# Kernel optimization log

Hardware: AMD Instinct MI355X
Metric: run time of the kernel (lower is better)

The kernel has to match this reference:

```python
import jax, jax.numpy as jnp
import numpy as np

# Loihi CUBA LIF neuron constants (netParams['neuron'])
V_TH_MANT = 80.0
THETA = V_TH_MANT * 64.0          # threshold in voltage units (vThMant << 6)
I_DECAY = 1024.0
V_DECAY = 128.0
REF_DELAY = 1.0
DECAY_U = 1.0 - I_DECAY / 4096.0  # current decay per step
DECAY_V = 1.0 - V_DECAY / 4096.0  # voltage decay per step
TAU_RHO = 1.0
SCALE_RHO = 1.0
POOL_W = 1.1 * V_TH_MANT          # SLAYER pool weight: one input spike -> 1.1*theta drive


@jax.custom_vjp
def spike_fn(v):
    # Heaviside spike with SLAYER surrogate gradient
    return (v >= THETA).astype(v.dtype)

def _spike_fwd(v):
    return spike_fn(v), v

def _spike_bwd(v, g):
    sur = (SCALE_RHO / THETA) * jnp.exp(-jnp.abs(v - THETA) / (TAU_RHO * THETA))
    return (g * sur,)

spike_fn.defvjp(_spike_fwd, _spike_bwd)


def spike_loihi(x):
    """Loihi LIF recurrence over last (time) axis. x: [..., T] weighted spikes."""
    shp = x.shape
    xt = jnp.moveaxis(x.reshape(-1, shp[-1]), -1, 0)  # [T, N]
    z = jnp.zeros(xt.shape[1], x.dtype)
    def step(carry, x_t):
        u, v, ref = carry
        u = u * DECAY_U + x_t * 64.0                  # current state (input scaled by 2^6)
        active = (ref <= 0).astype(x.dtype)
        v = (v * DECAY_V + u) * active                # voltage, clamped in refractory period
        s = spike_fn(v)
        ref = jnp.where(s > 0, REF_DELAY, jnp.maximum(ref - 1.0, 0.0))
        v = v * (1.0 - s)                             # reset on spike
        return (u, v, ref), s
    _, spikes = jax.lax.scan(step, (z, z, z), xt)
    return jnp.moveaxis(spikes, 0, -1).reshape(shp)


def delay_shift(x, d=1):
    # shift spikes forward in time by d steps (zero-pad at t=0)
    return jnp.pad(x, [(0, 0)] * (x.ndim - 1) + [(d, 0)])[..., :x.shape[-1]]


def conv2d_t(x, w):
    # x: [B,C,H,W,T], w: [O,I,k,k]; 2D 'SAME' conv applied independently per timestep
    B, C, H, W, T = x.shape
    xm = jnp.moveaxis(x, -1, 1).reshape(B * T, C, H, W)
    y = jax.lax.conv_general_dilated(xm, w, (1, 1), 'SAME',
                                     dimension_numbers=('NCHW', 'OIHW', 'NCHW'))
    O = w.shape[0]
    return jnp.moveaxis(y.reshape(B, T, O, H, W), 1, -1)


def sum_pool(x, k):
    # SLAYER pool = sum over kxk window * fixed weight (per timestep)
    y = jax.lax.reduce_window(x, 0.0, jax.lax.add,
                              (1, 1, k, k, 1), (1, 1, k, k, 1), 'VALID')
    return y * POOL_W


def setup_inputs() -> dict:
    key = jax.random.key(0)
    ks = jax.random.split(key, 5)
    B, T = 8, 128
    x = (jax.random.uniform(ks[0], (B, 2, 128, 128, T)) < 0.1).astype(jnp.float32)
    w1 = jax.random.normal(ks[1], (16, 2, 5, 5), jnp.float32) * 10.0 * 0.2   # weightScale=10
    w2 = jax.random.normal(ks[2], (32, 16, 3, 3), jnp.float32) * 50.0 * 0.2  # weightScale=50
    wf1 = jax.random.normal(ks[3], (512, 2048), jnp.float32) * 100.0 * 0.02  # dense default scale
    wf2 = jax.random.normal(ks[4], (11, 512), jnp.float32) * 100.0 * 0.02
    return {"x": x, "w1": w1, "w2": w2, "wf1": wf1, "wf2": wf2}


def reference(x, w1, w2, wf1, wf2):
    s = spike_loihi(sum_pool(x, 4))            # [B,2,32,32,T]
    s = delay_shift(s)
    s = spike_loihi(conv2d_t(s, w1))           # [B,16,32,32,T]
    s = delay_shift(s)
    s = spike_loihi(sum_pool(s, 2))            # [B,16,16,16,T]
    s = delay_shift(s)
    s = spike_loihi(conv2d_t(s, w2))           # [B,32,16,16,T]
    s = delay_shift(s)
    s = spike_loihi(sum_pool(s, 2))            # [B,32,8,8,T]
    B, T = s.shape[0], s.shape[-1]
    s = s.reshape(B, -1, T)                    # [B,2048,T]
    s = delay_shift(s)
    s = spike_loihi(jnp.einsum('bft,of->bot', s, wf1))  # [B,512,T]
    s = delay_shift(s)
    s = spike_loihi(jnp.einsum('bft,of->bot', s, wf2))  # [B,11,T]
    s = delay_shift(s)
    return s[:, :, None, None, :]              # [B,11,1,1,T]
```

## Files before the change

### kernel.cpp

```cpp
#include <hip/hip_runtime.h>

#define TT 128

#define DECAY_U 0.75f
#define DECAY_V 0.96875f
#define THETA   5120.0f
#define POOLW   88.0f

__device__ __forceinline__ void lif_step(float xt, float& u, float& v, int& refc, float& s) {
    u = __fadd_rn(__fmul_rn(u, DECAY_U), __fmul_rn(xt, 64.0f));
    float vn = __fadd_rn(__fmul_rn(v, DECAY_V), u);
    v = refc ? 0.0f : vn;
    s = (v >= THETA) ? 1.0f : 0.0f;
    if (s > 0.f) { refc = 1; v = 0.f; }
    else         { refc = refc > 0 ? refc - 1 : 0; }
}

__device__ __forceinline__ void lif_seq_lds(float* col, int stride) {
    float u = 0.f, v = 0.f;
    int refc = 0;
    #pragma unroll 16
    for (int t = 0; t < TT; ++t) {
        float s;
        lif_step(col[t * stride], u, v, refc, s);
        col[t * stride] = s;
    }
}

__global__ void wtrans_k(const float* __restrict__ w1, const float* __restrict__ w2,
                         float* __restrict__ wT1, float* __restrict__ wT2) {
    int i = blockIdx.x * 256 + threadIdx.x;
    if (i < 800) {
        int oc = i & 15;
        int r2 = i >> 4;
        int ky = r2 / 10;
        int rr = r2 - ky * 10;
        int kx = rr >> 1, c = rr & 1;
        wT1[i] = w1[oc*50 + c*25 + ky*5 + kx];
    }
    if (i < 4608) {
        int oc = i & 31;
        int c  = (i >> 5) & 15;
        int tap = i >> 9;
        wT2[i] = w2[oc*144 + c*9 + tap];
    }
}

__global__ void pool1_lif_k(const float* __restrict__ x, unsigned char* __restrict__ pk1) {
    __shared__ float sb[TT][3];
    int t = threadIdx.x & 127, c = threadIdx.x >> 7;
    int pos = blockIdx.x & 1023, b = blockIdx.x >> 10;
    int px = pos & 31, py = pos >> 5;
    const float* base = x + (size_t)((((b*2 + c)*128 + py*4)*128) + px*4) * 128 + t;
    float s = 0.f;
    #pragma unroll
    for (int dy = 0; dy < 4; ++dy)
        #pragma unroll
        for (int dx = 0; dx < 4; ++dx)
            s += base[(dy*128 + dx) * 128];
    sb[t][c] = s * POOLW;
    __syncthreads();
    if (threadIdx.x < 2) lif_seq_lds(&sb[0][threadIdx.x], 3);
    __syncthreads();
    if (threadIdx.x < 128) {
        unsigned int v = (sb[t][0] > 0.5f ? 1u : 0u) | (sb[t][1] > 0.5f ? 2u : 0u);
        pk1[(size_t)b * 131072 + (size_t)pos * 128 + t] = (unsigned char)v;
    }
}

__global__ __launch_bounds__(256) void conv1_gemm_k(const unsigned char* __restrict__ pk1,
                                                    const float* __restrict__ wT1,
                                                    unsigned short* __restrict__ pk2) {
    __shared__ float smem[4760];
    float* WS = smem;
    unsigned int* XN = (unsigned int*)(smem + 800);
    float* sb = smem;
    int tid = threadIdx.x;
    int ppair = blockIdx.x & 511, b = blockIdx.x >> 9;
    int py = ppair >> 4, px0 = (ppair & 15) * 2;
    const unsigned char* pp = pk1 + (size_t)b * 131072;

    #pragma unroll
    for (int i = 0; i < 4; ++i) {
        int e = tid + 256*i;
        if (e < 800) WS[e] = wT1[e];
    }
    #pragma unroll
    for (int i = 0; i < 15; ++i) {
        int e = tid + 256*i;
        int row = e >> 7, t = e & 127;
        int ky = row / 6, xc = row - ky*6;
        int iy = py + ky - 2, ix = px0 + xc - 2;
        bool vs = ((unsigned)iy < 32u) && ((unsigned)ix < 32u) && (t > 0);
        XN[row*132 + t] = vs ? (unsigned int)pp[(iy*32 + ix)*128 + t - 1] : 0u;
    }
    __syncthreads();

    int tg = tid & 31;
    int pos = (tid >> 5) & 1;
    int og = tid >> 6;
    float acc[4][4];
    #pragma unroll
    for (int i = 0; i < 4; ++i)
        #pragma unroll
        for (int j = 0; j < 4; ++j) acc[i][j] = 0.f;

    #pragma unroll 1
    for (int ky = 0; ky < 5; ++ky) {
        #pragma unroll
        for (int kx = 0; kx < 5; ++kx) {
            uint4 xw = *(const uint4*)&XN[(ky*6 + kx + pos)*132 + tg*4];
            #pragma unroll
            for (int c = 0; c < 2; ++c) {
                float4 wv = *(const float4*)&WS[(ky*10 + kx*2 + c)*16 + og*4];
                float x0 = (float)((xw.x >> c) & 1u);
                float x1 = (float)((xw.y >> c) & 1u);
                float x2 = (float)((xw.z >> c) & 1u);
                float x3 = (float)((xw.w >> c) & 1u);
                acc[0][0] = fmaf(wv.x, x0, acc[0][0]);
                acc[0][1] = fmaf(wv.x, x1, acc[0][1]);
                acc[0][2] = fmaf(wv.x, x2, acc[0][2]);
                acc[0][3] = fmaf(wv.x, x3, acc[0][3]);
                acc[1][0] = fmaf(wv.y, x0, acc[1][0]);
                acc[1][1] = fmaf(wv.y, x1, acc[1][1]);
                acc[1][2] = fmaf(wv.y, x2, acc[1][2]);
                acc[1][3] = fmaf(wv.y, x3, acc[1][3]);
                acc[2][0] = fmaf(wv.z, x0, acc[2][0]);
                acc[2][1] = fmaf(wv.z, x1, acc[2][1]);
                acc[2][2] = fmaf(wv.z, x2, acc[2][2]);
                acc[2][3] = fmaf(wv.z, x3, acc[2][3]);
                acc[3][0] = fmaf(wv.w, x0, acc[3][0]);
                acc[3][1] = fmaf(wv.w, x1, acc[3][1]);
                acc[3][2] = fmaf(wv.w, x2, acc[3][2]);
                acc[3][3] = fmaf(wv.w, x3, acc[3][3]);
            }
        }
    }
    __syncthreads();
    #pragma unroll
    for (int i = 0; i < 4; ++i)
        #pragma unroll
        for (int j = 0; j < 4; ++j)
            sb[(tg*4 + j)*33 + (og*4 + i)*2 + pos] = acc[i][j];
    __syncthreads();
    if (tid < 32) lif_seq_lds(&sb[tid], 33);
    __syncthreads();
    if (tid < 128) {
        int t = tid;
        #pragma unroll
        for (int p2 = 0; p2 < 2; ++p2) {
            unsigned int w = 0;
            #pragma unroll
            for (int oc = 0; oc < 16; ++oc)
                w |= (sb[t*33 + oc*2 + p2] > 0.5f ? 1u : 0u) << oc;
            int pos_out = py*32 + px0 + p2;
            pk2[(size_t)b * 131072 + (size_t)pos_out * 128 + t] = (unsigned short)w;
        }
    }
}

__global__ __launch_bounds__(256) void pool2pack_k(const unsigned short* __restrict__ pk2,
                                                   unsigned short* __restrict__ pk3) {
    __shared__ float sb[TT][17];
    int tid = threadIdx.x;
    int t = tid & 127, half = tid >> 7;
    int pos = blockIdx.x & 255, b = blockIdx.x >> 8;
    int px = pos & 15, py = pos >> 4;
    unsigned int w0 = 0, w1 = 0, w2 = 0, w3 = 0;
    if (t > 0) {
        const unsigned short* q = pk2 + (size_t)b * 131072 + (size_t)(py*2*32 + px*2) * 128 + (t - 1);
        w0 = q[0]; w1 = q[128]; w2 = q[32*128]; w3 = q[33*128];
    }
    #pragma unroll
    for (int j = 0; j < 8; ++j) {
        int c = half*8 + j;
        int cnt = ((w0 >> c) & 1) + ((w1 >> c) & 1) + ((w2 >> c) & 1) + ((w3 >> c) & 1);
        sb[t][c] = POOLW * (float)cnt;
    }
    __syncthreads();
    if (tid < 16) lif_seq_lds(&sb[0][tid], 17);
    __syncthreads();
    if (tid < 128) {
        unsigned int w = 0;
        #pragma unroll
        for (int c = 0; c < 16; ++c)
            w |= (sb[tid][c] > 0.5f ? 1u : 0u) << c;
        pk3[(size_t)b * 32768 + (size_t)pos * 128 + tid] = (unsigned short)w;
    }
}

__global__ __launch_bounds__(256) void conv2_gemm_k(const unsigned short* __restrict__ pk3,
                                                    const float* __restrict__ wT2,
                                                    unsigned int* __restrict__ pk4) {
    __shared__ float smem[5796];
    float* WS = smem;
    unsigned int* XL = (unsigned int*)(smem + 4608);
    float* sb = smem;
    int tid = threadIdx.x;
    int pos = blockIdx.x & 255, b = blockIdx.x >> 8;
    int px = pos & 15, py = pos >> 4;
    const unsigned short* pp = pk3 + (size_t)b * 32768;

    #pragma unroll
    for (int i = 0; i < 18; ++i)
        WS[tid + 256*i] = wT2[tid + 256*i];
    #pragma unroll
    for (int i = 0; i < 5; ++i) {
        int e = tid + 256*i;
        if (e < 1152) {
            int tap = e >> 7, t = e & 127;
            int ky = tap / 3, kx = tap - ky*3;
            int iy = py + ky - 1, ix = px + kx - 1;
            bool vs = ((unsigned)iy < 16u) && ((unsigned)ix < 16u) && (t > 0);
            XL[tap*132 + t] = vs ? (unsigned int)pp[(iy*16 + ix)*128 + t - 1] : 0u;
        }
    }
    __syncthreads();

    int tg = tid & 31;
    int og = tid >> 5;
    float acc[4][4];
    #pragma unroll
    for (int i = 0; i < 4; ++i)
        #pragma unroll
        for (int j = 0; j < 4; ++j) acc[i][j] = 0.f;

    #pragma unroll 1
    for (int tap = 0; tap < 9; ++tap) {
        uint4 xw = *(const uint4*)&XL[tap*132 + tg*4];
        #pragma unroll
        for (int c = 0; c < 16; ++c) {
            float4 wv = *(const float4*)&WS[tap*512 + c*32 + og*4];
            float x0 = (float)((xw.x >> c) & 1u);
            float x1 = (float)((xw.y >> c) & 1u);
            float x2 = (float)((xw.z >> c) & 1u);
            float x3 = (float)((xw.w >> c) & 1u);
            acc[0][0] = fmaf(wv.x, x0, acc[0][0]);
            acc[0][1] = fmaf(wv.x, x1, acc[0][1]);
            acc[0][2] = fmaf(wv.x, x2, acc[0][2]);
            acc[0][3] = fmaf(wv.x, x3, acc[0][3]);
            acc[1][0] = fmaf(wv.y, x0, acc[1][0]);
            acc[1][1] = fmaf(wv.y, x1, acc[1][1]);
            acc[1][2] = fmaf(wv.y, x2, acc[1][2]);
            acc[1][3] = fmaf(wv.y, x3, acc[1][3]);
            acc[2][0] = fmaf(wv.z, x0, acc[2][0]);
            acc[2][1] = fmaf(wv.z, x1, acc[2][1]);
            acc[2][2] = fmaf(wv.z, x2, acc[2][2]);
            acc[2][3] = fmaf(wv.z, x3, acc[2][3]);
            acc[3][0] = fmaf(wv.w, x0, acc[3][0]);
            acc[3][1] = fmaf(wv.w, x1, acc[3][1]);
            acc[3][2] = fmaf(wv.w, x2, acc[3][2]);
            acc[3][3] = fmaf(wv.w, x3, acc[3][3]);
        }
    }
    __syncthreads();
    #pragma unroll
    for (int i = 0; i < 4; ++i)
        #pragma unroll
        for (int j = 0; j < 4; ++j)
            sb[(tg*4 + j)*33 + og*4 + i] = acc[i][j];
    __syncthreads();
    if (tid < 32) lif_seq_lds(&sb[tid], 33);
    __syncthreads();
    if (tid < 128) {
        unsigned int w = 0;
        #pragma unroll
        for (int oc = 0; oc < 32; ++oc)
            w |= (sb[tid*33 + oc] > 0.5f ? 1u : 0u) << oc;
        pk4[(size_t)b * 32768 + (size_t)pos * 128 + tid] = w;
    }
}

__global__ void pool3_lif_k(const unsigned int* __restrict__ pk4, float* __restrict__ s5) {
    __shared__ float sb[TT][3];
    int t = threadIdx.x & 127, pos = threadIdx.x >> 7;
    int n = blockIdx.x * 2 + pos;
    int px = n & 7, py = (n >> 3) & 7, c = (n >> 6) & 31, b = n >> 11;
    float acc = 0.f;
    if (t > 0) {
        const unsigned int* q = pk4 + (size_t)b * 32768 + (size_t)(py*2*16 + px*2) * 128 + (t - 1);
        unsigned int w0 = q[0], w1 = q[128], w2 = q[16*128], w3 = q[17*128];
        int cnt = ((w0 >> c) & 1) + ((w1 >> c) & 1) + ((w2 >> c) & 1) + ((w3 >> c) & 1);
        acc = POOLW * (float)cnt;
    }
    sb[t][pos] = acc;
    __syncthreads();
    if (threadIdx.x < 2) lif_seq_lds(&sb[0][threadIdx.x], 3);
    __syncthreads();
    s5[(size_t)n * TT + t] = sb[t][pos];
}

__global__ __launch_bounds__(256) void fc1_gemm_k(const float* __restrict__ s5,
                                                  const float* __restrict__ wf1,
                                                  float* __restrict__ part) {
    __shared__ float WT[64][68];
    __shared__ float ST[64][68];
    int bid = blockIdx.x;
    int kc = bid & 7;
    int ot = (bid >> 3) & 7;
    int tt = (bid >> 6) & 1;
    int b  = bid >> 7;
    int tid = threadIdx.x;
    int oo = tid >> 4;
    int to = tid & 15;

    const float* wbase = wf1 + (size_t)(ot*64) * 2048 + kc*256;
    const float* sbase = s5 + (size_t)b * 262144 + (size_t)(kc*256) * 128;

    float acc[4][4];
    #pragma unroll
    for (int i = 0; i < 4; ++i)
        #pragma unroll
        for (int j = 0; j < 4; ++j) acc[i][j] = 0.f;

    for (int ks = 0; ks < 4; ++ks) {
        __syncthreads();
        #pragma unroll
        for (int i = 0; i < 16; ++i) {
            int e = tid + 256*i;
            int o = e >> 6, f = e & 63;
            WT[f][o] = wbase[(size_t)o * 2048 + ks*64 + f];
        }
        #pragma unroll
        for (int i = 0; i < 16; ++i) {
            int e = tid + 256*i;
            int f = e >> 6, tl = e & 63;
            int tsrc = tt*64 + tl - 1;
            ST[f][tl] = (tsrc < 0) ? 0.f : sbase[(size_t)f * 128 + ks*64*128 + tsrc];
        }
        __syncthreads();
        #pragma unroll 4
        for (int k = 0; k < 64; ++k) {
            float4 a = *(const float4*)&WT[k][oo*4];
            float4 s = *(const float4*)&ST[k][to*4];
            acc[0][0] = fmaf(a.x, s.x, acc[0][0]);
            acc[0][1] = fmaf(a.x, s.y, acc[0][1]);
            acc[0][2] = fmaf(a.x, s.z, acc[0][2]);
            acc[0][3] = fmaf(a.x, s.w, acc[0][3]);
            acc[1][0] = fmaf(a.y, s.x, acc[1][0]);
            acc[1][1] = fmaf(a.y, s.y, acc[1][1]);
            acc[1][2] = fmaf(a.y, s.z, acc[1][2]);
            acc[1][3] = fmaf(a.y, s.w, acc[1][3]);
            acc[2][0] = fmaf(a.z, s.x, acc[2][0]);
            acc[2][1] = fmaf(a.z, s.y, acc[2][1]);
            acc[2][2] = fmaf(a.z, s.z, acc[2][2]);
            acc[2][3] = fmaf(a.z, s.w, acc[2][3]);
            acc[3][0] = fmaf(a.w, s.x, acc[3][0]);
            acc[3][1] = fmaf(a.w, s.y, acc[3][1]);
            acc[3][2] = fmaf(a.w, s.z, acc[3][2]);
            acc[3][3] = fmaf(a.w, s.w, acc[3][3]);
        }
    }
    float* pb = part + (size_t)kc * 524288 + (size_t)b * 65536
              + (size_t)(ot*64 + oo*4) * 128 + tt*64 + to*4;
    #pragma unroll
    for (int i = 0; i < 4; ++i)
        #pragma unroll
        for (int j = 0; j < 4; ++j)
            pb[(size_t)i * 128 + j] = acc[i][j];
}

__global__ void fc1_reduce_lif_k(const float* __restrict__ part, float* __restrict__ s6) {
    __shared__ float sb[TT][3];
    int t = threadIdx.x & 127, pos = threadIdx.x >> 7;
    int n = blockIdx.x * 2 + pos;
    float s = 0.f;
    #pragma unroll
    for (int kc = 0; kc < 8; ++kc)
        s += part[(size_t)kc * 524288 + (size_t)n * 128 + t];
    sb[t][pos] = s;
    __syncthreads();
    if (threadIdx.x < 2) lif_seq_lds(&sb[0][threadIdx.x], 3);
    __syncthreads();
    s6[(size_t)n * TT + t] = sb[t][pos];
}

__global__ void fc2_lif_k(const float* __restrict__ s6, const float* __restrict__ wf2,
                          float* __restrict__ out) {
    __shared__ float sb[TT];
    int t = threadIdx.x;
    int o = blockIdx.x % 11, b = blockIdx.x / 11;
    float acc = 0.f;
    if (t > 0) {
        const float* sp = s6 + (size_t)b * 65536 + (t - 1);
        const float* wp = wf2 + o * 512;
        for (int f = 0; f < 512; f += 4) {
            float4 w = *(const float4*)&wp[f];
            acc = fmaf(w.x, sp[(size_t)f * 128], acc);
            acc = fmaf(w.y, sp[(size_t)(f+1) * 128], acc);
            acc = fmaf(w.z, sp[(size_t)(f+2) * 128], acc);
            acc = fmaf(w.w, sp[(size_t)(f+3) * 128], acc);
        }
    }
    sb[t] = acc;
    __syncthreads();
    if (t == 0) lif_seq_lds(sb, 1);
    __syncthreads();
    float* q = out + (size_t)(b*11 + o) * TT;
    if (t == 0) q[0] = 0.f;
    if (t < TT - 1) q[t + 1] = sb[t];
}

extern "C" void kernel_launch(void* const* d_in, const int* in_sizes, int n_in,
                              void* d_out, int out_size, void* d_ws, size_t ws_size,
                              hipStream_t stream) {
    const float* x   = (const float*)d_in[0];
    const float* w1  = (const float*)d_in[1];
    const float* w2  = (const float*)d_in[2];
    const float* wf1 = (const float*)d_in[3];
    const float* wf2 = (const float*)d_in[4];
    float* out = (float*)d_out;

    float* ws = (float*)d_ws;
    float* PART = ws;
    float* A    = PART + 4194304;
    float* S6   = A + 2097152;
    float* WT1  = S6 + 524288;
    float* WT2  = WT1 + 800;
    unsigned char*  PK1 = (unsigned char*)(WT2 + 4608);
    unsigned short* PK2 = (unsigned short*)(PK1 + 1048576);
    unsigned short* PK3 = (unsigned short*)((char*)PK2 + 2097152);
    unsigned int*   PK4 = (unsigned int*)((char*)PK3 + 524288);

    wtrans_k<<<dim3(18), 256, 0, stream>>>(w1, w2, WT1, WT2);
    pool1_lif_k<<<dim3(8192), 256, 0, stream>>>(x, PK1);
    conv1_gemm_k<<<dim3(4096), 256, 0, stream>>>(PK1, WT1, PK2);
    pool2pack_k<<<dim3(2048), 256, 0, stream>>>(PK2, PK3);
    conv2_gemm_k<<<dim3(2048), 256, 0, stream>>>(PK3, WT2, PK4);
    pool3_lif_k<<<dim3(8192), 256, 0, stream>>>(PK4, A);
    fc1_gemm_k      <<<dim3(1024), 256, 0, stream>>>(A, wf1, PART);
    fc1_reduce_lif_k<<<dim3(2048), 256, 0, stream>>>(PART, S6);
    fc2_lif_k<<<dim3(88), 128, 0, stream>>>(S6, wf2, out);
}
```

Baseline: 213.5 us.

## Process two output positions per conv2 block and fully unroll tap loops

The conv2 kernel now computes two spatial positions per block, halving the grid. Each thread accumulates 8 output channels instead of 4, and the staged weight tile is reused across both positions. The LIF scan runs on 64 threads instead of 32. The tap loops in conv1 and conv2 are now fully unrolled. The intent is to amortise the per-block weight load into LDS and add ILP, at the cost of more registers (32 accumulators) and more shared memory per block, which may lower occupancy.

```diff
diff --git a/kernel.cpp b/kernel.cpp
--- a/kernel.cpp
+++ b/kernel.cpp
@@ -105,7 +105,7 @@
         #pragma unroll
         for (int j = 0; j < 4; ++j) acc[i][j] = 0.f;
 
-    #pragma unroll 1
+    #pragma unroll
     for (int ky = 0; ky < 5; ++ky) {
         #pragma unroll
         for (int kx = 0; kx < 5; ++kx) {
@@ -192,82 +192,107 @@
 __global__ __launch_bounds__(256) void conv2_gemm_k(const unsigned short* __restrict__ pk3,
                                                     const float* __restrict__ wT2,
                                                     unsigned int* __restrict__ pk4) {
-    __shared__ float smem[5796];
+    __shared__ float smem[8448];
     float* WS = smem;
     unsigned int* XL = (unsigned int*)(smem + 4608);
     float* sb = smem;
     int tid = threadIdx.x;
-    int pos = blockIdx.x & 255, b = blockIdx.x >> 8;
-    int px = pos & 15, py = pos >> 4;
+    int pp2 = blockIdx.x & 127, b = blockIdx.x >> 7;
     const unsigned short* pp = pk3 + (size_t)b * 32768;
 
     #pragma unroll
     for (int i = 0; i < 18; ++i)
         WS[tid + 256*i] = wT2[tid + 256*i];
     #pragma unroll
-    for (int i = 0; i < 5; ++i) {
+    for (int i = 0; i < 9; ++i) {
         int e = tid + 256*i;
-        if (e < 1152) {
-            int tap = e >> 7, t = e & 127;
-            int ky = tap / 3, kx = tap - ky*3;
-            int iy = py + ky - 1, ix = px + kx - 1;
-            bool vs = ((unsigned)iy < 16u) && ((unsigned)ix < 16u) && (t > 0);
-            XL[tap*132 + t] = vs ? (unsigned int)pp[(iy*16 + ix)*128 + t - 1] : 0u;
-        }
+        int pe2 = e >= 1152 ? 1 : 0;
+        int r = e - pe2*1152;
+        int tap = r >> 7, t = r & 127;
+        int pos_l = pp2*2 + pe2;
+        int px = pos_l & 15, py = pos_l >> 4;
+        int ky = tap / 3, kx = tap - ky*3;
+        int iy = py + ky - 1, ix = px + kx - 1;
+        bool vs = ((unsigned)iy < 16u) && ((unsigned)ix < 16u) && (t > 0);
+        XL[pe2*1188 + tap*132 + t] = vs ? (unsigned int)pp[(iy*16 + ix)*128 + t - 1] : 0u;
     }
     __syncthreads();
 
     int tg = tid & 31;
-    int og = tid >> 5;
-    float acc[4][4];
-    #pragma unroll
-    for (int i = 0; i < 4; ++i)
+    int og = (tid >> 5) & 3;
+    int pe = tid >> 7;
+    const unsigned int* XLp = XL + pe*1188;
+    float acc[8][4];
+    #pragma unroll
+    for (int i = 0; i < 8; ++i)
         #pragma unroll
         for (int j = 0; j < 4; ++j) acc[i][j] = 0.f;
 
-    #pragma unroll 1
+    #pragma unroll
     for (int tap = 0; tap < 9; ++tap) {
-        uint4 xw = *(const uint4*)&XL[tap*132 + tg*4];
+        uint4 xw = *(const uint4*)&XLp[tap*132 + tg*4];
         #pragma unroll
         for (int c = 0; c < 16; ++c) {
-            float4 wv = *(const float4*)&WS[tap*512 + c*32 + og*4];
+            float4 wv0 = *(const float4*)&WS[tap*512 + c*32 + og*8];
+            float4 wv1 = *(const float4*)&WS[tap*512 + c*32 + og*8 + 4];
             float x0 = (float)((xw.x >> c) & 1u);
             float x1 = (float)((xw.y >> c) & 1u);
             float x2 = (float)((xw.z >> c) & 1u);
             float x3 = (float)((xw.w >> c) & 1u);
-            acc[0][0] = fmaf(wv.x, x0, acc[0][0]);
-            acc[0][1] = fmaf(wv.x, x1, acc[0][1]);
-            acc[0][2] = fmaf(wv.x, x2, acc[0][2]);
-            acc[0][3] = fmaf(wv.x, x3, acc[0][3]);
-            acc[1][0] = fmaf(wv.y, x0, acc[1][0]);
-            acc[1][1] = fmaf(wv.y, x1, acc[1][1]);
-            acc[1][2] = fmaf(wv.y, x2, acc[1][2]);
-            acc[1][3] = fmaf(wv.y, x3, acc[1][3]);
-            acc[2][0] = fmaf(wv.z, x0, acc[2][0]);
-            acc[2][1] = fmaf(wv.z, x1, acc[2][1]);
-            acc[2][2] = fmaf(wv.z, x2, acc[2][2]);
-            acc[2][3] = fmaf(wv.z, x3, acc[2][3]);
-            acc[3][0] = fmaf(wv.w, x0, acc[3][0]);
-            acc[3][1] = fmaf(wv.w, x1, acc[3][1]);
-            acc[3][2] = fmaf(wv.w, x2, acc[3][2]);
-            acc[3][3] = fmaf(wv.w, x3, acc[3][3]);
-        }
-    }
-    __syncthreads();
-    #pragma unroll
-    for (int i = 0; i < 4; ++i)
+            acc[0][0] = fmaf(wv0.x, x0, acc[0][0]);
+            acc[0][1] = fmaf(wv0.x, x1, acc[0][1]);
+            acc[0][2] = fmaf(wv0.x, x2, acc[0][2]);
+            acc[0][3] = fmaf(wv0.x, x3, acc[0][3]);
+            acc[1][0] = fmaf(wv0.y, x0, acc[1][0]);
+            acc[1][1] = fmaf(wv0.y, x1, acc[1][1]);
+            acc[1][2] = fmaf(wv0.y, x2, acc[1][2]);
+            acc[1][3] = fmaf(wv0.y, x3, acc[1][3]);
+            acc[2][0] = fmaf(wv0.z, x0, acc[2][0]);
+            acc[2][1] = fmaf(wv0.z, x1, acc[2][1]);
+            acc[2][2] = fmaf(wv0.z, x2, acc[2][2]);
+            acc[2][3] = fmaf(wv0.z, x3, acc[2][3]);
+            acc[3][0] = fmaf(wv0.w, x0, acc[3][0]);
+            acc[3][1] = fmaf(wv0.w, x1, acc[3][1]);
+            acc[3][2] = fmaf(wv0.w, x2, acc[3][2]);
+            acc[3][3] = fmaf(wv0.w, x3, acc[3][3]);
+            acc[4][0] = fmaf(wv1.x, x0, acc[4][0]);
+            acc[4][1] = fmaf(wv1.x, x1, acc[4][1]);
+            acc[4][2] = fmaf(wv1.x, x2, acc[4][2]);
+            acc[4][3] = fmaf(wv1.x, x3, acc[4][3]);
+            acc[5][0] = fmaf(wv1.y, x0, acc[5][0]);
+            acc[5][1] = fmaf(wv1.y, x1, acc[5][1]);
+            acc[5][2] = fmaf(wv1.y, x2, acc[5][2]);
+            acc[5][3] = fmaf(wv1.y, x3, acc[5][3]);
+            acc[6][0] = fmaf(wv1.z, x0, acc[6][0]);
+            acc[6][1] = fmaf(wv1.z, x1, acc[6][1]);
+            acc[6][2] = fmaf(wv1.z, x2, acc[6][2]);
+            acc[6][3] = fmaf(wv1.z, x3, acc[6][3]);
+            acc[7][0] = fmaf(wv1.w, x0, acc[7][0]);
+            acc[7][1] = fmaf(wv1.w, x1, acc[7][1]);
+            acc[7][2] = fmaf(wv1.w, x2, acc[7][2]);
+            acc[7][3] = fmaf(wv1.w, x3, acc[7][3]);
+        }
+    }
+    __syncthreads();
+    float* sbp = sb + pe*4224;
+    #pragma unroll
+    for (int i = 0; i < 8; ++i)
         #pragma unroll
         for (int j = 0; j < 4; ++j)
-            sb[(tg*4 + j)*33 + og*4 + i] = acc[i][j];
-    __syncthreads();
-    if (tid < 32) lif_seq_lds(&sb[tid], 33);
-    __syncthreads();
-    if (tid < 128) {
+            sbp[(tg*4 + j)*33 + og*8 + i] = acc[i][j];
+    __syncthreads();
+    if (tid < 64) {
+        int pe_l = tid >> 5, oc_l = tid & 31;
+        lif_seq_lds(&sb[pe_l*4224 + oc_l], 33);
+    }
+    __syncthreads();
+    {
+        int t = tid & 127, pe_l = tid >> 7;
         unsigned int w = 0;
         #pragma unroll
         for (int oc = 0; oc < 32; ++oc)
-            w |= (sb[tid*33 + oc] > 0.5f ? 1u : 0u) << oc;
-        pk4[(size_t)b * 32768 + (size_t)pos * 128 + tid] = w;
+            w |= (sb[pe_l*4224 + t*33 + oc] > 0.5f ? 1u : 0u) << oc;
+        pk4[(size_t)b * 32768 + (size_t)(pp2*2 + pe_l) * 128 + t] = w;
     }
 }
 
@@ -426,7 +451,7 @@
     pool1_lif_k<<<dim3(8192), 256, 0, stream>>>(x, PK1);
     conv1_gemm_k<<<dim3(4096), 256, 0, stream>>>(PK1, WT1, PK2);
     pool2pack_k<<<dim3(2048), 256, 0, stream>>>(PK2, PK3);
-    conv2_gemm_k<<<dim3(2048), 256, 0, stream>>>(PK3, WT2, PK4);
+    conv2_gemm_k<<<dim3(1024), 256, 0, stream>>>(PK3, WT2, PK4);
     pool3_lif_k<<<dim3(8192), 256, 0, stream>>>(PK4, A);
     fc1_gemm_k      <<<dim3(1024), 256, 0, stream>>>(A, wf1, PART);
     fc1_reduce_lif_k<<<dim3(2048), 256, 0, stream>>>(PART, S6);
```

Result: faster. 203.1 us (-4.9%).

## Replace binary-spike conv GEMMs with precomputed weight-sum lookup tables

Applied to the files above, without the earlier changes.

Because the conv inputs are binary spikes, the change precomputes per-row (conv1, 10 bits) and per-tap-half (conv2, 8 bits) partial weight sums for every input bit pattern. Each thread then gathers these table rows and adds them instead of running bit-extract plus FMA loops over all channels and taps. This removes most of the arithmetic in both conv kernels. In exchange it adds a LUT build kernel, random gathers into an L2-resident table of roughly 900 KB, higher register pressure, and a different float summation order that can flip spikes near threshold.

```diff
diff --git a/kernel.cpp b/kernel.cpp
--- a/kernel.cpp
+++ b/kernel.cpp
@@ -27,22 +27,33 @@
     }
 }
 
-__global__ void wtrans_k(const float* __restrict__ w1, const float* __restrict__ w2,
-                         float* __restrict__ wT1, float* __restrict__ wT2) {
-    int i = blockIdx.x * 256 + threadIdx.x;
-    if (i < 800) {
-        int oc = i & 15;
-        int r2 = i >> 4;
-        int ky = r2 / 10;
-        int rr = r2 - ky * 10;
-        int kx = rr >> 1, c = rr & 1;
-        wT1[i] = w1[oc*50 + c*25 + ky*5 + kx];
-    }
-    if (i < 4608) {
-        int oc = i & 31;
-        int c  = (i >> 5) & 15;
-        int tap = i >> 9;
-        wT2[i] = w2[oc*144 + c*9 + tap];
+__global__ void lut_build_k(const float* __restrict__ w1, const float* __restrict__ w2,
+                            float* __restrict__ LUT1, float* __restrict__ LUT2) {
+    int id = blockIdx.x * 256 + threadIdx.x;
+    if (id < 81920) {
+        int ky = id >> 14;
+        int idx = (id >> 4) & 1023;
+        int oc = id & 15;
+        float s = 0.f;
+        #pragma unroll
+        for (int j = 0; j < 10; ++j)
+            if ((idx >> j) & 1) {
+                int kx = j >> 1, c = j & 1;
+                s += w1[oc*50 + c*25 + ky*5 + kx];
+            }
+        LUT1[id] = s;
+    }
+    if (id < 147456) {
+        int th = id >> 13;
+        int idx = (id >> 5) & 255;
+        int oc = id & 31;
+        int tap = th >> 1, half = th & 1;
+        float s = 0.f;
+        #pragma unroll
+        for (int j = 0; j < 8; ++j)
+            if ((idx >> j) & 1)
+                s += w2[oc*144 + (half*8 + j)*9 + tap];
+        LUT2[id] = s;
     }
 }
 
@@ -68,94 +79,57 @@
     }
 }
 
-__global__ __launch_bounds__(256) void conv1_gemm_k(const unsigned char* __restrict__ pk1,
-                                                    const float* __restrict__ wT1,
-                                                    unsigned short* __restrict__ pk2) {
-    __shared__ float smem[4760];
-    float* WS = smem;
-    unsigned int* XN = (unsigned int*)(smem + 800);
-    float* sb = smem;
-    int tid = threadIdx.x;
-    int ppair = blockIdx.x & 511, b = blockIdx.x >> 9;
-    int py = ppair >> 4, px0 = (ppair & 15) * 2;
+__global__ __launch_bounds__(128) void conv1_lut_k(const unsigned char* __restrict__ pk1,
+                                                   const float* __restrict__ LUT1,
+                                                   unsigned short* __restrict__ pk2) {
+    __shared__ float sb[TT*17];
+    int t = threadIdx.x;
+    int pos = blockIdx.x & 1023, b = blockIdx.x >> 10;
+    int px = pos & 31, py = pos >> 5;
     const unsigned char* pp = pk1 + (size_t)b * 131072;
 
-    #pragma unroll
-    for (int i = 0; i < 4; ++i) {
-        int e = tid + 256*i;
-        if (e < 800) WS[e] = wT1[e];
-    }
-    #pragma unroll
-    for (int i = 0; i < 15; ++i) {
-        int e = tid + 256*i;
-        int row = e >> 7, t = e & 127;
-        int ky = row / 6, xc = row - ky*6;
-        int iy = py + ky - 2, ix = px0 + xc - 2;
-        bool vs = ((unsigned)iy < 32u) && ((unsigned)ix < 32u) && (t > 0);
-        XN[row*132 + t] = vs ? (unsigned int)pp[(iy*32 + ix)*128 + t - 1] : 0u;
-    }
-    __syncthreads();
-
-    int tg = tid & 31;
-    int pos = (tid >> 5) & 1;
-    int og = tid >> 6;
-    float acc[4][4];
-    #pragma unroll
-    for (int i = 0; i < 4; ++i)
-        #pragma unroll
-        for (int j = 0; j < 4; ++j) acc[i][j] = 0.f;
-
-    #pragma unroll 1
+    unsigned int idx[5];
+    #pragma unroll
     for (int ky = 0; ky < 5; ++ky) {
+        int iy = py + ky - 2;
+        unsigned int v = 0;
         #pragma unroll
         for (int kx = 0; kx < 5; ++kx) {
-            uint4 xw = *(const uint4*)&XN[(ky*6 + kx + pos)*132 + tg*4];
-            #pragma unroll
-            for (int c = 0; c < 2; ++c) {
-                float4 wv = *(const float4*)&WS[(ky*10 + kx*2 + c)*16 + og*4];
-                float x0 = (float)((xw.x >> c) & 1u);
-                float x1 = (float)((xw.y >> c) & 1u);
-                float x2 = (float)((xw.z >> c) & 1u);
-                float x3 = (float)((xw.w >> c) & 1u);
-                acc[0][0] = fmaf(wv.x, x0, acc[0][0]);
-                acc[0][1] = fmaf(wv.x, x1, acc[0][1]);
-                acc[0][2] = fmaf(wv.x, x2, acc[0][2]);
-                acc[0][3] = fmaf(wv.x, x3, acc[0][3]);
-                acc[1][0] = fmaf(wv.y, x0, acc[1][0]);
-                acc[1][1] = fmaf(wv.y, x1, acc[1][1]);
-                acc[1][2] = fmaf(wv.y, x2, acc[1][2]);
-                acc[1][3] = fmaf(wv.y, x3, acc[1][3]);
-                acc[2][0] = fmaf(wv.z, x0, acc[2][0]);
-                acc[2][1] = fmaf(wv.z, x1, acc[2][1]);
-                acc[2][2] = fmaf(wv.z, x2, acc[2][2]);
-                acc[2][3] = fmaf(wv.z, x3, acc[2][3]);
-                acc[3][0] = fmaf(wv.w, x0, acc[3][0]);
-                acc[3][1] = fmaf(wv.w, x1, acc[3][1]);
-                acc[3][2] = fmaf(wv.w, x2, acc[3][2]);
-                acc[3][3] = fmaf(wv.w, x3, acc[3][3]);
-            }
-        }
-    }
-    __syncthreads();
-    #pragma unroll
-    for (int i = 0; i < 4; ++i)
-        #pragma unroll
-        for (int j = 0; j < 4; ++j)
-            sb[(tg*4 + j)*33 + (og*4 + i)*2 + pos] = acc[i][j];
-    __syncthreads();
-    if (tid < 32) lif_seq_lds(&sb[tid], 33);
-    __syncthreads();
-    if (tid < 128) {
-        int t = tid;
-        #pragma unroll
-        for (int p2 = 0; p2 < 2; ++p2) {
-            unsigned int w = 0;
-            #pragma unroll
-            for (int oc = 0; oc < 16; ++oc)
-                w |= (sb[t*33 + oc*2 + p2] > 0.5f ? 1u : 0u) << oc;
-            int pos_out = py*32 + px0 + p2;
-            pk2[(size_t)b * 131072 + (size_t)pos_out * 128 + t] = (unsigned short)w;
-        }
+            int ix = px + kx - 2;
+            bool vs = ((unsigned)iy < 32u) && ((unsigned)ix < 32u) && (t > 0);
+            unsigned int nb = vs ? (unsigned int)pp[(iy*32 + ix)*128 + t - 1] : 0u;
+            v |= nb << (kx*2);
+        }
+        idx[ky] = v;
+    }
+
+    float acc[16];
+    #pragma unroll
+    for (int k = 0; k < 16; ++k) acc[k] = 0.f;
+    #pragma unroll
+    for (int ky = 0; ky < 5; ++ky) {
+        const float4* Lp = (const float4*)(LUT1 + (size_t)(ky*1024 + idx[ky]) * 16);
+        #pragma unroll
+        for (int q = 0; q < 4; ++q) {
+            float4 l = Lp[q];
+            acc[q*4+0] += l.x;
+            acc[q*4+1] += l.y;
+            acc[q*4+2] += l.z;
+            acc[q*4+3] += l.w;
+        }
+    }
+
+    #pragma unroll
+    for (int oc = 0; oc < 16; ++oc) sb[t*17 + oc] = acc[oc];
+    __syncthreads();
+    if (t < 16) lif_seq_lds(&sb[t], 17);
+    __syncthreads();
+    {
+        unsigned int w = 0;
+        #pragma unroll
+        for (int oc = 0; oc < 16; ++oc)
+            w |= (sb[t*17 + oc] > 0.5f ? 1u : 0u) << oc;
+        pk2[(size_t)b * 131072 + (size_t)pos * 128 + t] = (unsigned short)w;
     }
 }
 
@@ -189,85 +163,60 @@
     }
 }
 
-__global__ __launch_bounds__(256) void conv2_gemm_k(const unsigned short* __restrict__ pk3,
-                                                    const float* __restrict__ wT2,
-                                                    unsigned int* __restrict__ pk4) {
-    __shared__ float smem[5796];
-    float* WS = smem;
-    unsigned int* XL = (unsigned int*)(smem + 4608);
-    float* sb = smem;
-    int tid = threadIdx.x;
+__global__ __launch_bounds__(128) void conv2_lut_k(const unsigned short* __restrict__ pk3,
+                                                   const float* __restrict__ LUT2,
+                                                   unsigned int* __restrict__ pk4) {
+    __shared__ float sb[TT*33];
+    int t = threadIdx.x;
     int pos = blockIdx.x & 255, b = blockIdx.x >> 8;
     int px = pos & 15, py = pos >> 4;
     const unsigned short* pp = pk3 + (size_t)b * 32768;
 
-    #pragma unroll
-    for (int i = 0; i < 18; ++i)
-        WS[tid + 256*i] = wT2[tid + 256*i];
-    #pragma unroll
-    for (int i = 0; i < 5; ++i) {
-        int e = tid + 256*i;
-        if (e < 1152) {
-            int tap = e >> 7, t = e & 127;
-            int ky = tap / 3, kx = tap - ky*3;
-            int iy = py + ky - 1, ix = px + kx - 1;
-            bool vs = ((unsigned)iy < 16u) && ((unsigned)ix < 16u) && (t > 0);
-            XL[tap*132 + t] = vs ? (unsigned int)pp[(iy*16 + ix)*128 + t - 1] : 0u;
-        }
-    }
-    __syncthreads();
-
-    int tg = tid & 31;
-    int og = tid >> 5;
-    float acc[4][4];
-    #pragma unroll
-    for (int i = 0; i < 4; ++i)
-        #pragma unroll
-        for (int j = 0; j < 4; ++j) acc[i][j] = 0.f;
-
-    #pragma unroll 1
+    unsigned int wv[9];
+    #pragma unroll
     for (int tap = 0; tap < 9; ++tap) {
-        uint4 xw = *(const uint4*)&XL[tap*132 + tg*4];
-        #pragma unroll
-        for (int c = 0; c < 16; ++c) {
-            float4 wv = *(const float4*)&WS[tap*512 + c*32 + og*4];
-            float x0 = (float)((xw.x >> c) & 1u);
-            float x1 = (float)((xw.y >> c) & 1u);
-            float x2 = (float)((xw.z >> c) & 1u);
-            float x3 = (float)((xw.w >> c) & 1u);
-            acc[0][0] = fmaf(wv.x, x0, acc[0][0]);
-            acc[0][1] = fmaf(wv.x, x1, acc[0][1]);
-            acc[0][2] = fmaf(wv.x, x2, acc[0][2]);
-            acc[0][3] = fmaf(wv.x, x3, acc[0][3]);
-            acc[1][0] = fmaf(wv.y, x0, acc[1][0]);
-            acc[1][1] = fmaf(wv.y, x1, acc[1][1]);
-            acc[1][2] = fmaf(wv.y, x2, acc[1][2]);
-            acc[1][3] = fmaf(wv.y, x3, acc[1][3]);
-            acc[2][0] = fmaf(wv.z, x0, acc[2][0]);
-            acc[2][1] = fmaf(wv.z, x1, acc[2][1]);
-            acc[2][2] = fmaf(wv.z, x2, acc[2][2]);
-            acc[2][3] = fmaf(wv.z, x3, acc[2][3]);
-            acc[3][0] = fmaf(wv.w, x0, acc[3][0]);
-            acc[3][1] = fmaf(wv.w, x1, acc[3][1]);
-            acc[3][2] = fmaf(wv.w, x2, acc[3][2]);
-            acc[3][3] = fmaf(wv.w, x3, acc[3][3]);
-        }
-    }
-    __syncthreads();
-    #pragma unroll
-    for (int i = 0; i < 4; ++i)
-        #pragma unroll
-        for (int j = 0; j < 4; ++j)
-            sb[(tg*4 + j)*33 + og*4 + i] = acc[i][j];
-    __syncthreads();
-    if (tid < 32) lif_seq_lds(&sb[tid], 33);
-    __syncthreads();
-    if (tid < 128) {
+        int ky = tap / 3, kx = tap - ky*3;
+        int iy = py + ky - 1, ix = px + kx - 1;
+        bool vs = ((unsigned)iy < 16u) && ((unsigned)ix < 16u) && (t > 0);
+        wv[tap] = vs ? (unsigned int)pp[(iy*16 + ix)*128 + t - 1] : 0u;
+    }
+
+    float acc[32];
+    #pragma unroll
+    for (int k = 0; k < 32; ++k) acc[k] = 0.f;
+    #pragma unroll
+    for (int tap = 0; tap < 9; ++tap) {
+        const float4* p0 = (const float4*)(LUT2 + (size_t)((tap*2 + 0)*256 + (wv[tap] & 255u)) * 32);
+        #pragma unroll
+        for (int q = 0; q < 8; ++q) {
+            float4 l = p0[q];
+            acc[q*4+0] += l.x;
+            acc[q*4+1] += l.y;
+            acc[q*4+2] += l.z;
+            acc[q*4+3] += l.w;
+        }
+        const float4* p1 = (const float4*)(LUT2 + (size_t)((tap*2 + 1)*256 + ((wv[tap] >> 8) & 255u)) * 32);
+        #pragma unroll
+        for (int q = 0; q < 8; ++q) {
+            float4 l = p1[q];
+            acc[q*4+0] += l.x;
+            acc[q*4+1] += l.y;
+            acc[q*4+2] += l.z;
+            acc[q*4+3] += l.w;
+        }
+    }
+
+    #pragma unroll
+    for (int oc = 0; oc < 32; ++oc) sb[t*33 + oc] = acc[oc];
+    __syncthreads();
+    if (t < 32) lif_seq_lds(&sb[t], 33);
+    __syncthreads();
+    {
         unsigned int w = 0;
         #pragma unroll
         for (int oc = 0; oc < 32; ++oc)
-            w |= (sb[tid*33 + oc] > 0.5f ? 1u : 0u) << oc;
-        pk4[(size_t)b * 32768 + (size_t)pos * 128 + tid] = w;
+            w |= (sb[t*33 + oc] > 0.5f ? 1u : 0u) << oc;
+        pk4[(size_t)b * 32768 + (size_t)pos * 128 + t] = w;
     }
 }
 
@@ -415,18 +364,18 @@
     float* PART = ws;
     float* A    = PART + 4194304;
     float* S6   = A + 2097152;
-    float* WT1  = S6 + 524288;
-    float* WT2  = WT1 + 800;
-    unsigned char*  PK1 = (unsigned char*)(WT2 + 4608);
+    float* LUT1 = S6 + 524288;
+    float* LUT2 = LUT1 + 81920;
+    unsigned char*  PK1 = (unsigned char*)(LUT2 + 147456);
     unsigned short* PK2 = (unsigned short*)(PK1 + 1048576);
     unsigned short* PK3 = (unsigned short*)((char*)PK2 + 2097152);
     unsigned int*   PK4 = (unsigned int*)((char*)PK3 + 524288);
 
-    wtrans_k<<<dim3(18), 256, 0, stream>>>(w1, w2, WT1, WT2);
+    lut_build_k<<<dim3(576), 256, 0, stream>>>(w1, w2, LUT1, LUT2);
     pool1_lif_k<<<dim3(8192), 256, 0, stream>>>(x, PK1);
-    conv1_gemm_k<<<dim3(4096), 256, 0, stream>>>(PK1, WT1, PK2);
+    conv1_lut_k<<<dim3(8192), 128, 0, stream>>>(PK1, LUT1, PK2);
     pool2pack_k<<<dim3(2048), 256, 0, stream>>>(PK2, PK3);
-    conv2_gemm_k<<<dim3(2048), 256, 0, stream>>>(PK3, WT2, PK4);
+    conv2_lut_k<<<dim3(2048), 128, 0, stream>>>(PK3, LUT2, PK4);
     pool3_lif_k<<<dim3(8192), 256, 0, stream>>>(PK4, A);
     fc1_gemm_k      <<<dim3(1024), 256, 0, stream>>>(A, wf1, PART);
     fc1_reduce_lif_k<<<dim3(2048), 256, 0, stream>>>(PART, S6);
```

New measurement: 205.9 us. 3.6% less time.
